# Kernel optimization log

Measured on AMD Instinct MI355X. Metric: run time of the kernel, lower is better.

Reference implementation:

```python
import jax, jax.numpy as jnp
import numpy as np

# BlendParams defaults (pytorch3d)
SIGMA = 1e-4
GAMMA = 1e-4
BG_BLUE = 1.0       # background_color = (1,1,1); module returns channel 2
ZNEAR = 1.0
ZFAR = 100.0
EPS = 1e-10

N, H, W, K = 8, 256, 256, 50


def setup_inputs() -> dict:
    key = jax.random.key(0)
    k1, k2, k3 = jax.random.split(key, 3)
    # depth buffer values in [znear, zfar]
    zbuf = jax.random.uniform(k1, (N, H, W, K), dtype=jnp.float32) * (ZFAR - ZNEAR) + ZNEAR
    # signed (squared) pixel-to-edge distances: small magnitudes near 0
    dists = jax.random.normal(k2, (N, H, W, K), dtype=jnp.float32) * 1e-3
    # face indices; -1 marks empty slots (~1/100000 here, plus explicit tail masking)
    pix_to_face = jax.random.randint(k3, (N, H, W, K), -1, 100000, dtype=jnp.int64)
    # make the last few K-slots empty, as a real rasterizer would
    slot = jnp.arange(K)
    pix_to_face = jnp.where(slot < K - 5, pix_to_face, jnp.int64(-1))
    return {"zbuf": zbuf, "dists": dists, "pix_to_face": pix_to_face}


def reference(zbuf, dists, pix_to_face):
    # softmax_rgb_blend with colors == zbuf broadcast over 3 channels;
    # the module returns images[..., 2] (blue channel of the blended RGBA).
    mask = (pix_to_face >= 0).astype(zbuf.dtype)                      # (N,H,W,K)
    prob = jax.nn.sigmoid(-dists / SIGMA) * mask                      # distance sigmoid
    # z-based softmax weights (stabilized by per-pixel max)
    z_inv = (ZFAR - zbuf) / (ZFAR - ZNEAR) * mask                     # (N,H,W,K)
    z_inv_max = jnp.maximum(jnp.max(z_inv, axis=-1, keepdims=True), EPS)
    weights_num = prob * jnp.exp((z_inv - z_inv_max) / GAMMA)         # (N,H,W,K)
    delta = jnp.maximum(jnp.exp((EPS - z_inv_max) / GAMMA), EPS)      # (N,H,W,1)
    denom = jnp.sum(weights_num, axis=-1, keepdims=True) + delta      # (N,H,W,1)
    # weighted color sum; all three channels equal zbuf, take channel 2
    weighted = jnp.sum(weights_num * zbuf, axis=-1, keepdims=True)    # (N,H,W,1)
    blue = (weighted + delta * BG_BLUE) / denom                       # (N,H,W,1)
    return blue[..., 0]                                               # (N,H,W)
```

## Files before the change

kernel.cpp:

```cpp
#include <hip/hip_runtime.h>


constexpr int THREADS = 256;
constexpr int LPP     = 8;
constexpr int PPB     = THREADS / LPP;

constexpr float INV_SIGMA  = 1e4f;
constexpr float INVG       = 1e4f;
constexpr float ZFAR       = 100.0f;
constexpr float ZRANGE     = 99.0f;
constexpr float INV_ZRANGE = 1.0f / 99.0f;
constexpr float EPS        = 1e-10f;

__global__ __launch_bounds__(THREADS) void soft_depth_kernel(
    const float* __restrict__ zbuf,
    const float* __restrict__ dists,
    const int*   __restrict__ p2f,
    float*       __restrict__ out)
{
    const int t = threadIdx.x;
    const int q = t & (LPP - 1);
    const size_t pix = (size_t)blockIdx.x * PPB + (t >> 3);
    const size_t cb  = pix * 25;

    const float2* __restrict__ z2 = (const float2*)zbuf;
    const float2* __restrict__ d2 = (const float2*)dists;
    const int2*   __restrict__ f2 = (const int2*)p2f;

    const size_t c0 = cb + q, c1 = cb + q + 8, c2 = cb + q + 16, c3 = cb + 24;
    const float2 za = z2[c0], zb = z2[c1], zc = z2[c2], zd = z2[c3];
    const float2 da = d2[c0], db = d2[c1], dc = d2[c2], dd = d2[c3];
    const int2   fa = f2[c0], fb = f2[c1], fc = f2[c2], fd = f2[c3];

    float zv[8], pv[8];
    {
        const bool v3 = (q == 0);
        const bool m0 = (fa.x >= 0),       m1 = (fa.y >= 0);
        const bool m2 = (fb.x >= 0),       m3 = (fb.y >= 0);
        const bool m4 = (fc.x >= 0),       m5 = (fc.y >= 0);
        const bool m6 = v3 && (fd.x >= 0), m7 = v3 && (fd.y >= 0);
        zv[0] = m0 ? (ZFAR - za.x) * INV_ZRANGE : 0.0f;
        zv[1] = m1 ? (ZFAR - za.y) * INV_ZRANGE : 0.0f;
        zv[2] = m2 ? (ZFAR - zb.x) * INV_ZRANGE : 0.0f;
        zv[3] = m3 ? (ZFAR - zb.y) * INV_ZRANGE : 0.0f;
        zv[4] = m4 ? (ZFAR - zc.x) * INV_ZRANGE : 0.0f;
        zv[5] = m5 ? (ZFAR - zc.y) * INV_ZRANGE : 0.0f;
        zv[6] = m6 ? (ZFAR - zd.x) * INV_ZRANGE : 0.0f;
        zv[7] = m7 ? (ZFAR - zd.y) * INV_ZRANGE : 0.0f;
        pv[0] = m0 ? 1.0f / (1.0f + __expf(da.x * INV_SIGMA)) : 0.0f;
        pv[1] = m1 ? 1.0f / (1.0f + __expf(da.y * INV_SIGMA)) : 0.0f;
        pv[2] = m2 ? 1.0f / (1.0f + __expf(db.x * INV_SIGMA)) : 0.0f;
        pv[3] = m3 ? 1.0f / (1.0f + __expf(db.y * INV_SIGMA)) : 0.0f;
        pv[4] = m4 ? 1.0f / (1.0f + __expf(dc.x * INV_SIGMA)) : 0.0f;
        pv[5] = m5 ? 1.0f / (1.0f + __expf(dc.y * INV_SIGMA)) : 0.0f;
        pv[6] = m6 ? 1.0f / (1.0f + __expf(dd.x * INV_SIGMA)) : 0.0f;
        pv[7] = m7 ? 1.0f / (1.0f + __expf(dd.y * INV_SIGMA)) : 0.0f;
    }

    float m = fmaxf(fmaxf(fmaxf(zv[0], zv[1]), fmaxf(zv[2], zv[3])),
                    fmaxf(fmaxf(zv[4], zv[5]), fmaxf(zv[6], zv[7])));
    m = fmaxf(m, __shfl_xor(m, 1));
    m = fmaxf(m, __shfl_xor(m, 2));
    m = fmaxf(m, __shfl_xor(m, 4));
    m = fmaxf(m, EPS);

    float S1a = 0.0f, S1b = 0.0f, S2a = 0.0f, S2b = 0.0f;
    #pragma unroll
    for (int j = 0; j < 8; j += 2) {
        const float w0 = pv[j]   * __expf((zv[j]   - m) * INVG);
        const float w1 = pv[j+1] * __expf((zv[j+1] - m) * INVG);
        S1a += w0;
        S1b += w1;
        S2a += w0 * (ZFAR - zv[j]   * ZRANGE);
        S2b += w1 * (ZFAR - zv[j+1] * ZRANGE);
    }
    float S1 = S1a + S1b;
    float S2 = S2a + S2b;
    S1 += __shfl_xor(S1, 1);  S1 += __shfl_xor(S1, 2);  S1 += __shfl_xor(S1, 4);
    S2 += __shfl_xor(S2, 1);  S2 += __shfl_xor(S2, 2);  S2 += __shfl_xor(S2, 4);

    if (q == 0) {
        const float delta = fmaxf(__expf((EPS - m) * INVG), EPS);
        out[pix] = (S2 + delta) / (S1 + delta);
    }
}

extern "C" void kernel_launch(void* const* d_in, const int* in_sizes, int n_in,
                              void* d_out, int out_size, void* d_ws, size_t ws_size,
                              hipStream_t stream) {
    const float* zbuf  = (const float*)d_in[0];
    const float* dists = (const float*)d_in[1];
    const int*   p2f   = (const int*)d_in[2];
    float* out = (float*)d_out;

    const int pixels = out_size;
    const int blocks = pixels / PPB;

    soft_depth_kernel<<<dim3(blocks), dim3(THREADS), 0, stream>>>(
        zbuf, dists, p2f, out);
}
```

Measured before the change: 279.7 us.

## Process eight pixels per team with software-pipelined prefetch of next pixel

Each block now handles eight pixels per 8-lane team instead of one. The loads for the next pixel are issued before the current pixel is computed, so memory latency overlaps with the exp/reduction work. The grid shrinks eightfold, and launch bounds request 4 waves per SIMD. The cost is higher register pressure and fewer blocks, which could hurt occupancy for this bandwidth-bound kernel.

```diff
diff --git a/kernel.cpp b/kernel.cpp
--- a/kernel.cpp
+++ b/kernel.cpp
@@ -3,7 +3,9 @@
 
 constexpr int THREADS = 256;
 constexpr int LPP     = 8;
-constexpr int PPB     = THREADS / LPP;
+constexpr int TEAMS   = THREADS / LPP;
+constexpr int ITERS   = 8;
+constexpr int PPB     = TEAMS * ITERS;
 
 constexpr float INV_SIGMA  = 1e4f;
 constexpr float INVG       = 1e4f;
@@ -12,49 +14,52 @@
 constexpr float INV_ZRANGE = 1.0f / 99.0f;
 constexpr float EPS        = 1e-10f;
 
-__global__ __launch_bounds__(THREADS) void soft_depth_kernel(
-    const float* __restrict__ zbuf,
-    const float* __restrict__ dists,
-    const int*   __restrict__ p2f,
-    float*       __restrict__ out)
+struct Raw {
+    float2 za, zb, zc, zd;
+    float2 da, db, dc, dd;
+    int2   fa, fb, fc, fd;
+};
+
+__device__ __forceinline__ Raw load_pixel(const float2* __restrict__ z2,
+                                          const float2* __restrict__ d2,
+                                          const int2*   __restrict__ f2,
+                                          size_t pix, int q)
 {
-    const int t = threadIdx.x;
-    const int q = t & (LPP - 1);
-    const size_t pix = (size_t)blockIdx.x * PPB + (t >> 3);
-    const size_t cb  = pix * 25;
+    const size_t cb = pix * 25;
+    const size_t c0 = cb + q, c1 = cb + q + 8, c2 = cb + q + 16, c3 = cb + 24;
+    Raw r;
+    r.za = z2[c0]; r.zb = z2[c1]; r.zc = z2[c2]; r.zd = z2[c3];
+    r.da = d2[c0]; r.db = d2[c1]; r.dc = d2[c2]; r.dd = d2[c3];
+    r.fa = f2[c0]; r.fb = f2[c1]; r.fc = f2[c2]; r.fd = f2[c3];
+    return r;
+}
 
-    const float2* __restrict__ z2 = (const float2*)zbuf;
-    const float2* __restrict__ d2 = (const float2*)dists;
-    const int2*   __restrict__ f2 = (const int2*)p2f;
-
-    const size_t c0 = cb + q, c1 = cb + q + 8, c2 = cb + q + 16, c3 = cb + 24;
-    const float2 za = z2[c0], zb = z2[c1], zc = z2[c2], zd = z2[c3];
-    const float2 da = d2[c0], db = d2[c1], dc = d2[c2], dd = d2[c3];
-    const int2   fa = f2[c0], fb = f2[c1], fc = f2[c2], fd = f2[c3];
-
+__device__ __forceinline__ void process_pixel(const Raw& r, int q,
+                                              float* __restrict__ out, size_t pix)
+{
     float zv[8], pv[8];
     {
         const bool v3 = (q == 0);
-        const bool m0 = (fa.x >= 0),       m1 = (fa.y >= 0);
-        const bool m2 = (fb.x >= 0),       m3 = (fb.y >= 0);
-        const bool m4 = (fc.x >= 0),       m5 = (fc.y >= 0);
-        const bool m6 = v3 && (fd.x >= 0), m7 = v3 && (fd.y >= 0);
-        zv[0] = m0 ? (ZFAR - za.x) * INV_ZRANGE : 0.0f;
-        zv[1] = m1 ? (ZFAR - za.y) * INV_ZRANGE : 0.0f;
-        zv[2] = m2 ? (ZFAR - zb.x) * INV_ZRANGE : 0.0f;
-        zv[3] = m3 ? (ZFAR - zb.y) * INV_ZRANGE : 0.0f;
-        zv[4] = m4 ? (ZFAR - zc.x) * INV_ZRANGE : 0.0f;
-        zv[5] = m5 ? (ZFAR - zc.y) * INV_ZRANGE : 0.0f;
-        zv[6] = m6 ? (ZFAR - zd.x) * INV_ZRANGE : 0.0f;
-        zv[7] = m7 ? (ZFAR - zd.y) * INV_ZRANGE : 0.0f;
-        pv[0] = m0 ? 1.0f / (1.0f + __expf(da.x * INV_SIGMA)) : 0.0f;
-        pv[1] = m1 ? 1.0f / (1.0f + __expf(da.y * INV_SIGMA)) : 0.0f;
-        pv[2] = m2 ? 1.0f / (1.0f + __expf(db.x * INV_SIGMA)) : 0.0f;
-        pv[3] = m3 ? 1.0f / (1.0f + __expf(db.y * INV_SIGMA)) : 0.0f;
-        pv[4] = m4 ? 1.0f / (1.0f + __expf(dc.x * INV_SIGMA)) : 0.0f;
-        pv[5] = m5 ? 1.0f / (1.0f + __expf(dc.y * INV_SIGMA)) : 0.0f;
-        pv[6] = m6 ? 1.0f / (1.0f + __expf(dd.x * INV_SIGMA)) : 0.0f;
-        pv[7] = m7 ? 1.0f / (1.0f + __expf(dd.y * INV_SIGMA)) : 0.0f;
+        const bool m0 = (r.fa.x >= 0),       m1 = (r.fa.y >= 0);
+        const bool m2 = (r.fb.x >= 0),       m3 = (r.fb.y >= 0);
+        const bool m4 = (r.fc.x >= 0),       m5 = (r.fc.y >= 0);
+        const bool m6 = v3 && (r.fd.x >= 0), m7 = v3 && (r.fd.y >= 0);
+        zv[0] = m0 ? (ZFAR - r.za.x) * INV_ZRANGE : 0.0f;
+        zv[1] = m1 ? (ZFAR - r.za.y) * INV_ZRANGE : 0.0f;
+        zv[2] = m2 ? (ZFAR - r.zb.x) * INV_ZRANGE : 0.0f;
+        zv[3] = m3 ? (ZFAR - r.zb.y) * INV_ZRANGE : 0.0f;
+        zv[4] = m4 ? (ZFAR - r.zc.x) * INV_ZRANGE : 0.0f;
+        zv[5] = m5 ? (ZFAR - r.zc.y) * INV_ZRANGE : 0.0f;
+        zv[6] = m6 ? (ZFAR - r.zd.x) * INV_ZRANGE : 0.0f;
+        zv[7] = m7 ? (ZFAR - r.zd.y) * INV_ZRANGE : 0.0f;
+        pv[0] = m0 ? 1.0f / (1.0f + __expf(r.da.x * INV_SIGMA)) : 0.0f;
+        pv[1] = m1 ? 1.0f / (1.0f + __expf(r.da.y * INV_SIGMA)) : 0.0f;
+        pv[2] = m2 ? 1.0f / (1.0f + __expf(r.db.x * INV_SIGMA)) : 0.0f;
+        pv[3] = m3 ? 1.0f / (1.0f + __expf(r.db.y * INV_SIGMA)) : 0.0f;
+        pv[4] = m4 ? 1.0f / (1.0f + __expf(r.dc.x * INV_SIGMA)) : 0.0f;
+        pv[5] = m5 ? 1.0f / (1.0f + __expf(r.dc.y * INV_SIGMA)) : 0.0f;
+        pv[6] = m6 ? 1.0f / (1.0f + __expf(r.dd.x * INV_SIGMA)) : 0.0f;
+        pv[7] = m7 ? 1.0f / (1.0f + __expf(r.dd.y * INV_SIGMA)) : 0.0f;
     }
 
     float m = fmaxf(fmaxf(fmaxf(zv[0], zv[1]), fmaxf(zv[2], zv[3])),
@@ -85,6 +90,31 @@
     }
 }
 
+__global__ __launch_bounds__(THREADS, 4) void soft_depth_kernel(
+    const float* __restrict__ zbuf,
+    const float* __restrict__ dists,
+    const int*   __restrict__ p2f,
+    float*       __restrict__ out)
+{
+    const int t    = threadIdx.x;
+    const int q    = t & (LPP - 1);
+    const int team = t >> 3;
+    const size_t base = (size_t)blockIdx.x * PPB + team;
+
+    const float2* __restrict__ z2 = (const float2*)zbuf;
+    const float2* __restrict__ d2 = (const float2*)dists;
+    const int2*   __restrict__ f2 = (const int2*)p2f;
+
+    Raw cur = load_pixel(z2, d2, f2, base, q);
+    #pragma unroll
+    for (int j = 1; j < ITERS; ++j) {
+        Raw nxt = load_pixel(z2, d2, f2, base + (size_t)j * TEAMS, q);
+        process_pixel(cur, q, out, base + (size_t)(j - 1) * TEAMS);
+        cur = nxt;
+    }
+    process_pixel(cur, q, out, base + (size_t)(ITERS - 1) * TEAMS);
+}
+
 extern "C" void kernel_launch(void* const* d_in, const int* in_sizes, int n_in,
                               void* d_out, int out_size, void* d_ws, size_t ws_size,
                               hipStream_t stream) {
```

Measured after the change: 286.9 us. 1.03x slower.
